# Kernel tuning notes

Measured on AMD Instinct MI355X. Metric: run time of the kernel, lower is better.

## Reference

```python
import jax, jax.numpy as jnp
import numpy as np

COLLAPSE_FRAC = 4  # collapse F // 4 lowest-weight faces (target_size = 3/4 * F)


def setup_inputs() -> dict:
    key = jax.random.key(0)
    k1, k2, k3 = jax.random.split(key, 3)
    B, F, C, K = 8, 8192, 256, 4
    features = jax.random.normal(k1, (B, F, C), dtype=jnp.float32)
    adjacency = jax.random.randint(k2, (B, F, 3), 0, F).astype(jnp.int32)
    ring_k = jax.random.randint(k3, (B, F, K), 0, F).astype(jnp.int32)
    return {"features": features, "adjacency": adjacency, "ring_k": ring_k}


def _pool(features, adjacency, ring_k):
    # features:  [B, F, C] float   per-face features
    # adjacency: [B, F, 3] int     3 neighboring faces of each triangle
    # ring_k:    [B, F, K] int     k-ring neighborhood used for collapse weights
    B, F, C = features.shape
    K = ring_k.shape[-1]
    # ring-aggregated saliency weight per face (compute_weights analogue)
    rf = jnp.take_along_axis(
        features, ring_k.reshape(B, F * K)[:, :, None], axis=1
    ).reshape(B, F, K, C)                      # [B, F, K, C]
    w = jnp.linalg.norm(rf.mean(axis=2), axis=-1)  # [B, F]

    # select lowest-weight faces to collapse (idx/sorted analogue)
    P = F // COLLAPSE_FRAC
    _, collapse_idx = jax.lax.top_k(-w, P)      # [B, P]

    # gather the 3 region neighbors and the collapsed face features
    neighbors = jnp.take_along_axis(adjacency, collapse_idx[:, :, None], axis=1)  # [B, P, 3]
    cf = jnp.take_along_axis(features, collapse_idx[:, :, None], axis=1)          # [B, P, C]

    # scatter collapsed-face features into their 3 adjacent faces (update_features analogue)
    offs = (jnp.arange(B, dtype=jnp.int32) * F)[:, None, None]   # [B, 1, 1]
    seg = (neighbors + offs).reshape(-1)                          # [B*P*3]
    vals = jnp.broadcast_to(cf[:, :, None, :] / 3.0, (B, P, 3, C)).reshape(-1, C)
    scat = jax.ops.segment_sum(vals, seg, num_segments=B * F).reshape(B, F, C)
    cnt = jax.ops.segment_sum(
        jnp.ones(seg.shape, jnp.float32), seg, num_segments=B * F
    ).reshape(B, F, 1)
    merged = (features + scat) / (1.0 + cnt)

    # erase collapsed faces (erased / update_faces analogue; static shape, mask instead of compaction)
    erase_flat = (collapse_idx + offs[:, :, 0]).reshape(-1)
    keep = (
        jnp.ones((B * F,), jnp.float32).at[erase_flat].set(0.0).reshape(B, F, 1)
    )
    return merged * keep


def reference(features, adjacency, ring_k):
    return _pool(features, adjacency, ring_k)
```

## Files before the change

### kernel.cpp

```cpp
#include <hip/hip_runtime.h>
#include <stdint.h>

#define B 8
#define F 8192
#define C 256
#define K 4
#define P (F / 4)
#define CAP 16
#define NB 4096
#define NSLICE 4
#define MMB 8

__device__ __forceinline__ int binOf(float v, float lo, float scale) {
    int bin = (int)((v - lo) * scale);
    return bin < 0 ? 0 : (bin > NB - 1 ? NB - 1 : bin);
}

__device__ __forceinline__ void loScale(const unsigned int* bmn,
                                        const unsigned int* bmx,
                                        float& lo, float& scale) {
    unsigned int mn = 0xFFFFFFFFu, mx = 0u;
#pragma unroll
    for (int i = 0; i < MMB; ++i) {
        const unsigned int a = bmn[i], b = bmx[i];
        mn = mn < a ? mn : a;
        mx = mx > b ? mx : b;
    }
    lo = __uint_as_float(mn);
    const float hi = __uint_as_float(mx);
    scale = (float)(NB - 2) / fmaxf(hi - lo, 1e-30f);
}

__global__ __launch_bounds__(256) void kW(const float* __restrict__ feat,
                                          const int* __restrict__ ring,
                                          float* __restrict__ w,
                                          int* __restrict__ cnt,
                                          int* __restrict__ flag) {
    const int wid  = blockIdx.x * 4 + (threadIdx.x >> 6);
    const int lane = threadIdx.x & 63;
    const int b    = wid >> 13;

    const int rbase = wid * K;
    const int r0 = ring[rbase + 0], r1 = ring[rbase + 1];
    const int r2 = ring[rbase + 2], r3 = ring[rbase + 3];
    const float4* f4 = (const float4*)feat;
    const size_t base = (size_t)b * F;
    const int    CW   = C / 4;
    const float4 v0 = f4[(base + r0) * CW + lane];
    const float4 v1 = f4[(base + r1) * CW + lane];
    const float4 v2 = f4[(base + r2) * CW + lane];
    const float4 v3 = f4[(base + r3) * CW + lane];

    float4 a;
    a.x = (v0.x + v1.x) + (v2.x + v3.x);
    a.y = (v0.y + v1.y) + (v2.y + v3.y);
    a.z = (v0.z + v1.z) + (v2.z + v3.z);
    a.w = (v0.w + v1.w) + (v2.w + v3.w);
    float s = (a.x * a.x + a.y * a.y + a.z * a.z + a.w * a.w) * 0.0625f;
#pragma unroll
    for (int off = 32; off > 0; off >>= 1) s += __shfl_down(s, off, 64);
    if (lane == 0) {
        w[wid]    = sqrtf(s);
        cnt[wid]  = 0;
        flag[wid] = 0;
    }
}

__global__ __launch_bounds__(256) void kMM(const float* __restrict__ w,
                                           unsigned int* __restrict__ bmn,
                                           unsigned int* __restrict__ bmx) {
    __shared__ unsigned int smn[256], smx[256];
    unsigned int mn = 0xFFFFFFFFu, mx = 0u;
    for (int i = blockIdx.x * 256 + threadIdx.x; i < B * F; i += MMB * 256) {
        const unsigned int u = __float_as_uint(w[i]);
        mn = mn < u ? mn : u;
        mx = mx > u ? mx : u;
    }
    smn[threadIdx.x] = mn; smx[threadIdx.x] = mx;
    __syncthreads();
    for (int off = 128; off > 0; off >>= 1) {
        if (threadIdx.x < off) {
            smn[threadIdx.x] = min(smn[threadIdx.x], smn[threadIdx.x + off]);
            smx[threadIdx.x] = max(smx[threadIdx.x], smx[threadIdx.x + off]);
        }
        __syncthreads();
    }
    if (threadIdx.x == 0) { bmn[blockIdx.x] = smn[0]; bmx[blockIdx.x] = smx[0]; }
}

__global__ __launch_bounds__(256) void kH(const float* __restrict__ w,
                                          const unsigned int* __restrict__ bmn,
                                          const unsigned int* __restrict__ bmx,
                                          int* __restrict__ hist) {
    __shared__ int h[NB];
    for (int i = threadIdx.x; i < NB; i += 256) h[i] = 0;
    __syncthreads();
    float lo, scale;
    loScale(bmn, bmx, lo, scale);
    const int base = blockIdx.x * 2048;
#pragma unroll
    for (int k = 0; k < 8; ++k) {
        const float v = w[base + threadIdx.x + k * 256];
        atomicAdd(&h[binOf(v, lo, scale)], 1);
    }
    __syncthreads();
    int* slice = hist + (size_t)blockIdx.x * NB;
    for (int i = threadIdx.x; i < NB; i += 256) slice[i] = h[i];
}

__global__ __launch_bounds__(1024) void kT(const int* __restrict__ hist,
                                           int* __restrict__ tbin,
                                           int* __restrict__ trank,
                                           int* __restrict__ ccnt) {
    __shared__ int hb[NB];
    __shared__ int part[1024];
    const int b = blockIdx.x, t = threadIdx.x;
    if (t == 0) ccnt[b] = 0;
    const int* h0 = hist + (size_t)b * NSLICE * NB;
    int s = 0;
#pragma unroll
    for (int i = 0; i < 4; ++i) {
        const int bin = t * 4 + i;
        const int v = h0[bin] + h0[NB + bin] + h0[2 * NB + bin] + h0[3 * NB + bin];
        hb[bin] = v;
        s += v;
    }
    part[t] = s;
    __syncthreads();
    for (int off = 1; off < 1024; off <<= 1) {
        const int v = part[t];
        const int u = (t >= off) ? part[t - off] : 0;
        __syncthreads();
        part[t] = v + u;
        __syncthreads();
    }
    const int excl = (t == 0) ? 0 : part[t - 1];
    if (P - 1 >= excl && P - 1 < part[t]) {
        int c = excl;
#pragma unroll
        for (int i = 0; i < 4; ++i) {
            const int bin = t * 4 + i;
            const int hv = hb[bin];
            if (P - 1 < c + hv) { tbin[b] = bin; trank[b] = P - c; break; }
            c += hv;
        }
    }
}

__global__ __launch_bounds__(256) void kFL(const float* __restrict__ w,
                                           const int* __restrict__ adj,
                                           const unsigned int* __restrict__ bmn,
                                           const unsigned int* __restrict__ bmx,
                                           const int* __restrict__ tbin,
                                           int* __restrict__ flag,
                                           int* __restrict__ cnt,
                                           int* __restrict__ srcs,
                                           unsigned long long* __restrict__ cand,
                                           int* __restrict__ ccnt) {
    __shared__ unsigned long long lc[256];
    __shared__ int lcnt;
    __shared__ int lbase;
    if (threadIdx.x == 0) lcnt = 0;
    __syncthreads();

    float lo, scale;
    loScale(bmn, bmx, lo, scale);

    const int t = blockIdx.x * 256 + threadIdx.x;
    const int b = t >> 13;
    const float v = w[t];
    const int bin = binOf(v, lo, scale);
    const int T = tbin[b];
    if (bin < T) {
        flag[t] = 1;
#pragma unroll
        for (int j = 0; j < 3; ++j) {
            const int n    = adj[(size_t)t * 3 + j];
            const int tgt  = b * F + n;
            const int slot = atomicAdd(&cnt[tgt], 1);
            if (slot < CAP) srcs[(size_t)tgt * CAP + slot] = t;
        }
    } else if (bin == T) {
        const int pos = atomicAdd(&lcnt, 1);
        lc[pos] = ((unsigned long long)__float_as_uint(v) << 32) | (uint32_t)(t & (F - 1));
    }
    __syncthreads();
    if (threadIdx.x == 0 && lcnt > 0)
        lbase = atomicAdd(&ccnt[b], lcnt);
    __syncthreads();
    const int m = lcnt;
    for (int i = threadIdx.x; i < m; i += 256)
        cand[(size_t)b * F + lbase + i] = lc[i];
}

__global__ __launch_bounds__(1024) void kSel(const int* __restrict__ ccnt,
                                             const int* __restrict__ trank,
                                             const unsigned long long* __restrict__ cand,
                                             const int* __restrict__ adj,
                                             int* __restrict__ flag,
                                             int* __restrict__ cnt,
                                             int* __restrict__ srcs) {
    __shared__ unsigned long long keys[F];
    const int b = blockIdx.x;
    const int n = ccnt[b];
    const int R = trank[b];
    for (int i = threadIdx.x; i < n; i += 1024)
        keys[i] = cand[(size_t)b * F + i];
    __syncthreads();
    for (int i = threadIdx.x; i < n; i += 1024) {
        const unsigned long long my = keys[i];
        int rank = 0;
        for (int j = 0; j < n; ++j) rank += (keys[j] < my) ? 1 : 0;
        if (rank < R) {
            const int t = b * F + (int)(uint32_t)my;
            flag[t] = 1;
#pragma unroll
            for (int j = 0; j < 3; ++j) {
                const int nb   = adj[(size_t)t * 3 + j];
                const int tgt  = b * F + nb;
                const int slot = atomicAdd(&cnt[tgt], 1);
                if (slot < CAP) srcs[(size_t)tgt * CAP + slot] = t;
            }
        }
    }
}

__global__ __launch_bounds__(256) void kG(const float* __restrict__ feat,
                                          const int* __restrict__ cnt,
                                          const int* __restrict__ flag,
                                          const int* __restrict__ srcs,
                                          float* __restrict__ out) {
    const int wid  = blockIdx.x * 4 + (threadIdx.x >> 6);
    const int lane = threadIdx.x & 63;
    float4* drow = (float4*)(out + (size_t)wid * C);

    if (flag[wid]) {
        drow[lane] = make_float4(0.f, 0.f, 0.f, 0.f);
        return;
    }
    const int m  = cnt[wid];
    const int mm = m < CAP ? m : CAP;

    const int sidx = (lane < CAP) ? srcs[(size_t)wid * CAP + lane] : 0;

    float4 acc = ((const float4*)(feat + (size_t)wid * C))[lane];
    const float inv3 = 1.0f / 3.0f;
    for (int i = 0; i < mm; ++i) {
        const int s = __shfl(sidx, i, 64);
        const float4 v = ((const float4*)(feat + (size_t)s * C))[lane];
        acc.x += v.x * inv3; acc.y += v.y * inv3;
        acc.z += v.z * inv3; acc.w += v.w * inv3;
    }
    const float inv = 1.0f / (1.0f + (float)m);
    acc.x *= inv; acc.y *= inv; acc.z *= inv; acc.w *= inv;
    drow[lane] = acc;
}

extern "C" void kernel_launch(void* const* d_in, const int* in_sizes, int n_in,
                              void* d_out, int out_size, void* d_ws, size_t ws_size,
                              hipStream_t stream) {
    const float* feat = (const float*)d_in[0];
    const int*   adj  = (const int*)d_in[1];
    const int*   ring = (const int*)d_in[2];
    float* out = (float*)d_out;

    unsigned long long* cand = (unsigned long long*)d_ws;
    float* w     = (float*)(cand + B * F);
    int*   cnt   = (int*)(w + B * F);
    int*   flag  = cnt + B * F;
    int*   hist  = flag + B * F;
    int*   srcs  = hist + B * NSLICE * NB;
    int*   ccnt  = srcs + (size_t)B * F * CAP;
    int*   tbin  = ccnt + B;
    int*   trank = tbin + B;
    unsigned int* bmn = (unsigned int*)(trank + B);
    unsigned int* bmx = bmn + MMB;

    kW  <<<(B * F) / 4, 256, 0, stream>>>(feat, ring, w, cnt, flag);
    kMM <<<MMB, 256, 0, stream>>>(w, bmn, bmx);
    kH  <<<(B * F) / 2048, 256, 0, stream>>>(w, bmn, bmx, hist);
    kT  <<<B, 1024, 0, stream>>>(hist, tbin, trank, ccnt);
    kFL <<<(B * F) / 256, 256, 0, stream>>>(w, adj, bmn, bmx, tbin, flag, cnt, srcs, cand, ccnt);
    kSel<<<B, 1024, 0, stream>>>(ccnt, trank, cand, adj, flag, cnt, srcs);
    kG  <<<(B * F) / 4, 256, 0, stream>>>(feat, cnt, flag, srcs, out);
}
```

Measured before the change: 172.3 us.

## Fuse min/max, histogram and threshold kernels into one per-batch kernel

Replaces the global min/max, sliced histogram and threshold-scan kernels with a single per-batch kernel that computes per-batch min/max, builds the histogram in shared memory and finds the threshold bin. This removes two launches and the global histogram round-trip. Per-batch ranges replace the global range, so binning changes but stays valid. It also interleaves the block-to-batch mapping in kW and kG so blocks from every batch run at the same time.

```diff
diff --git a/kernel.cpp b/kernel.cpp
--- a/kernel.cpp
+++ b/kernel.cpp
@@ -8,27 +8,10 @@
 #define P (F / 4)
 #define CAP 16
 #define NB 4096
-#define NSLICE 4
-#define MMB 8
 
 __device__ __forceinline__ int binOf(float v, float lo, float scale) {
     int bin = (int)((v - lo) * scale);
     return bin < 0 ? 0 : (bin > NB - 1 ? NB - 1 : bin);
-}
-
-__device__ __forceinline__ void loScale(const unsigned int* bmn,
-                                        const unsigned int* bmx,
-                                        float& lo, float& scale) {
-    unsigned int mn = 0xFFFFFFFFu, mx = 0u;
-#pragma unroll
-    for (int i = 0; i < MMB; ++i) {
-        const unsigned int a = bmn[i], b = bmx[i];
-        mn = mn < a ? mn : a;
-        mx = mx > b ? mx : b;
-    }
-    lo = __uint_as_float(mn);
-    const float hi = __uint_as_float(mx);
-    scale = (float)(NB - 2) / fmaxf(hi - lo, 1e-30f);
 }
 
 __global__ __launch_bounds__(256) void kW(const float* __restrict__ feat,
@@ -36,9 +19,10 @@
                                           float* __restrict__ w,
                                           int* __restrict__ cnt,
                                           int* __restrict__ flag) {
-    const int wid  = blockIdx.x * 4 + (threadIdx.x >> 6);
-    const int lane = threadIdx.x & 63;
-    const int b    = wid >> 13;
+    const int b     = blockIdx.x & 7;
+    const int inner = blockIdx.x >> 3;
+    const int wid   = b * F + inner * 4 + (threadIdx.x >> 6);
+    const int lane  = threadIdx.x & 63;
 
     const int rbase = wid * K;
     const int r0 = ring[rbase + 0], r1 = ring[rbase + 1];
@@ -66,65 +50,55 @@
     }
 }
 
-__global__ __launch_bounds__(256) void kMM(const float* __restrict__ w,
-                                           unsigned int* __restrict__ bmn,
-                                           unsigned int* __restrict__ bmx) {
-    __shared__ unsigned int smn[256], smx[256];
+__global__ __launch_bounds__(1024) void kHT(const float* __restrict__ w,
+                                            int* __restrict__ tbin,
+                                            int* __restrict__ trank,
+                                            int* __restrict__ ccnt,
+                                            unsigned int* __restrict__ lsb) {
+    __shared__ int h[NB];
+    __shared__ unsigned int red[1024];
+    const int b = blockIdx.x, t = threadIdx.x;
+
+    float val[8];
     unsigned int mn = 0xFFFFFFFFu, mx = 0u;
-    for (int i = blockIdx.x * 256 + threadIdx.x; i < B * F; i += MMB * 256) {
-        const unsigned int u = __float_as_uint(w[i]);
+#pragma unroll
+    for (int k = 0; k < 8; ++k) {
+        val[k] = w[b * F + t + k * 1024];
+        const unsigned int u = __float_as_uint(val[k]);
         mn = mn < u ? mn : u;
         mx = mx > u ? mx : u;
     }
-    smn[threadIdx.x] = mn; smx[threadIdx.x] = mx;
-    __syncthreads();
-    for (int off = 128; off > 0; off >>= 1) {
-        if (threadIdx.x < off) {
-            smn[threadIdx.x] = min(smn[threadIdx.x], smn[threadIdx.x + off]);
-            smx[threadIdx.x] = max(smx[threadIdx.x], smx[threadIdx.x + off]);
-        }
-        __syncthreads();
-    }
-    if (threadIdx.x == 0) { bmn[blockIdx.x] = smn[0]; bmx[blockIdx.x] = smx[0]; }
-}
-
-__global__ __launch_bounds__(256) void kH(const float* __restrict__ w,
-                                          const unsigned int* __restrict__ bmn,
-                                          const unsigned int* __restrict__ bmx,
-                                          int* __restrict__ hist) {
-    __shared__ int h[NB];
-    for (int i = threadIdx.x; i < NB; i += 256) h[i] = 0;
-    __syncthreads();
-    float lo, scale;
-    loScale(bmn, bmx, lo, scale);
-    const int base = blockIdx.x * 2048;
-#pragma unroll
-    for (int k = 0; k < 8; ++k) {
-        const float v = w[base + threadIdx.x + k * 256];
-        atomicAdd(&h[binOf(v, lo, scale)], 1);
-    }
-    __syncthreads();
-    int* slice = hist + (size_t)blockIdx.x * NB;
-    for (int i = threadIdx.x; i < NB; i += 256) slice[i] = h[i];
-}
-
-__global__ __launch_bounds__(1024) void kT(const int* __restrict__ hist,
-                                           int* __restrict__ tbin,
-                                           int* __restrict__ trank,
-                                           int* __restrict__ ccnt) {
-    __shared__ int hb[NB];
-    __shared__ int part[1024];
-    const int b = blockIdx.x, t = threadIdx.x;
-    if (t == 0) ccnt[b] = 0;
-    const int* h0 = hist + (size_t)b * NSLICE * NB;
+    red[t] = mn;
+    __syncthreads();
+    for (int off = 512; off > 0; off >>= 1) {
+        if (t < off) red[t] = min(red[t], red[t + off]);
+        __syncthreads();
+    }
+    const unsigned int lob = red[0];
+    __syncthreads();
+    red[t] = mx;
+    __syncthreads();
+    for (int off = 512; off > 0; off >>= 1) {
+        if (t < off) red[t] = max(red[t], red[t + off]);
+        __syncthreads();
+    }
+    const unsigned int hib = red[0];
+    __syncthreads();
+
+    const float lo    = __uint_as_float(lob);
+    const float hi    = __uint_as_float(hib);
+    const float scale = (float)(NB - 2) / fmaxf(hi - lo, 1e-30f);
+
+    for (int i = t; i < NB; i += 1024) h[i] = 0;
+    __syncthreads();
+#pragma unroll
+    for (int k = 0; k < 8; ++k) atomicAdd(&h[binOf(val[k], lo, scale)], 1);
+    __syncthreads();
+
     int s = 0;
 #pragma unroll
-    for (int i = 0; i < 4; ++i) {
-        const int bin = t * 4 + i;
-        const int v = h0[bin] + h0[NB + bin] + h0[2 * NB + bin] + h0[3 * NB + bin];
-        hb[bin] = v;
-        s += v;
-    }
+    for (int i = 0; i < 4; ++i) s += h[t * 4 + i];
+    int* part = (int*)red;
     part[t] = s;
     __syncthreads();
     for (int off = 1; off < 1024; off <<= 1) {
@@ -140,17 +114,21 @@
 #pragma unroll
         for (int i = 0; i < 4; ++i) {
             const int bin = t * 4 + i;
-            const int hv = hb[bin];
+            const int hv = h[bin];
             if (P - 1 < c + hv) { tbin[b] = bin; trank[b] = P - c; break; }
             c += hv;
         }
     }
+    if (t == 0) {
+        ccnt[b] = 0;
+        lsb[b * 2 + 0] = lob;
+        lsb[b * 2 + 1] = hib;
+    }
 }
 
 __global__ __launch_bounds__(256) void kFL(const float* __restrict__ w,
                                            const int* __restrict__ adj,
-                                           const unsigned int* __restrict__ bmn,
-                                           const unsigned int* __restrict__ bmx,
+                                           const unsigned int* __restrict__ lsb,
                                            const int* __restrict__ tbin,
                                            int* __restrict__ flag,
                                            int* __restrict__ cnt,
@@ -163,11 +141,12 @@
     if (threadIdx.x == 0) lcnt = 0;
     __syncthreads();
 
-    float lo, scale;
-    loScale(bmn, bmx, lo, scale);
-
     const int t = blockIdx.x * 256 + threadIdx.x;
     const int b = t >> 13;
+    const float lo    = __uint_as_float(lsb[b * 2 + 0]);
+    const float hi    = __uint_as_float(lsb[b * 2 + 1]);
+    const float scale = (float)(NB - 2) / fmaxf(hi - lo, 1e-30f);
+
     const float v = w[t];
     const int bin = binOf(v, lo, scale);
     const int T = tbin[b];
@@ -230,8 +209,10 @@
                                           const int* __restrict__ flag,
                                           const int* __restrict__ srcs,
                                           float* __restrict__ out) {
-    const int wid  = blockIdx.x * 4 + (threadIdx.x >> 6);
-    const int lane = threadIdx.x & 63;
+    const int b     = blockIdx.x & 7;
+    const int inner = blockIdx.x >> 3;
+    const int wid   = b * F + inner * 4 + (threadIdx.x >> 6);
+    const int lane  = threadIdx.x & 63;
     float4* drow = (float4*)(out + (size_t)wid * C);
 
     if (flag[wid]) {
@@ -268,19 +249,15 @@
     float* w     = (float*)(cand + B * F);
     int*   cnt   = (int*)(w + B * F);
     int*   flag  = cnt + B * F;
-    int*   hist  = flag + B * F;
-    int*   srcs  = hist + B * NSLICE * NB;
+    int*   srcs  = flag + B * F;
     int*   ccnt  = srcs + (size_t)B * F * CAP;
     int*   tbin  = ccnt + B;
     int*   trank = tbin + B;
-    unsigned int* bmn = (unsigned int*)(trank + B);
-    unsigned int* bmx = bmn + MMB;
+    unsigned int* lsb = (unsigned int*)(trank + B);
 
     kW  <<<(B * F) / 4, 256, 0, stream>>>(feat, ring, w, cnt, flag);
-    kMM <<<MMB, 256, 0, stream>>>(w, bmn, bmx);
-    kH  <<<(B * F) / 2048, 256, 0, stream>>>(w, bmn, bmx, hist);
-    kT  <<<B, 1024, 0, stream>>>(hist, tbin, trank, ccnt);
-    kFL <<<(B * F) / 256, 256, 0, stream>>>(w, adj, bmn, bmx, tbin, flag, cnt, srcs, cand, ccnt);
+    kHT <<<B, 1024, 0, stream>>>(w, tbin, trank, ccnt, lsb);
+    kFL <<<(B * F) / 256, 256, 0, stream>>>(w, adj, lsb, tbin, flag, cnt, srcs, cand, ccnt);
     kSel<<<B, 1024, 0, stream>>>(ccnt, trank, cand, adj, flag, cnt, srcs);
     kG  <<<(B * F) / 4, 256, 0, stream>>>(feat, cnt, flag, srcs, out);
 }
```

Result: faster. 162.6 us (-5.7%).
